# Kernel tuning notes

Measured on AMD Instinct MI355X. Metric: run time of the kernel, lower is better.

Reference implementation:

```python
import jax, jax.numpy as jnp
import numpy as np

K = 100
TEMPERATURE = 1.0


def setup_inputs() -> dict:
    key = jax.random.key(0)
    k1, k2, k3 = jax.random.split(key, 3)
    student_emb = jax.random.normal(k1, (8, 512, 1500), dtype=jnp.float32)
    teacher_codes = jax.random.randint(k2, (8, 1500), 0, 4096, dtype=jnp.int64)
    codebook = jax.random.normal(k3, (4096, 512), dtype=jnp.float32)
    return {"student_emb": student_emb, "teacher_codes": teacher_codes, "codebook": codebook}


def reference(student_emb, teacher_codes, codebook):
    B, C, T = student_emb.shape
    # flatten tokens: (N, C) with N = B*T
    emb = jnp.transpose(student_emb, (0, 2, 1)).reshape(-1, C)
    codes = teacher_codes.reshape(-1).astype(jnp.int32)

    # Euclidean cdist via the ||a||^2 + ||b||^2 - 2ab expansion (same math as torch.cdist)
    emb_sq = jnp.sum(emb * emb, axis=1, keepdims=True)            # (N,1)
    cb_sq = jnp.sum(codebook * codebook, axis=1)[None, :]         # (1,V)
    d2 = emb_sq + cb_sq - 2.0 * jnp.matmul(emb, codebook.T)       # (N,V)
    distances = jnp.sqrt(jnp.maximum(d2, 0.0))

    # top-k smallest distances
    _, top_k_indices = jax.lax.top_k(-distances, K)               # (N,K)

    # include_correct: replace last candidate with the true code if absent
    correct_in_topk = jnp.any(top_k_indices == codes[:, None], axis=1)
    top_k_indices = top_k_indices.at[:, -1].set(
        jnp.where(correct_in_topk, top_k_indices[:, -1], codes))

    candidate_distances = jnp.take_along_axis(distances, top_k_indices, axis=1)
    logits = -candidate_distances / TEMPERATURE                   # (N,K)

    match = top_k_indices == codes[:, None]
    local_labels = jnp.argmax(match.astype(jnp.int32), axis=1)    # (N,)

    logp = jax.nn.log_softmax(logits, axis=1)
    loss = -jnp.mean(jnp.take_along_axis(logp, local_labels[:, None], axis=1))

    local_predictions = jnp.argmax(logits, axis=-1)
    local_accuracy = jnp.mean((local_predictions == local_labels).astype(jnp.float32))
    global_predictions = jnp.argmin(distances, axis=-1)
    global_accuracy = jnp.mean((global_predictions == codes).astype(jnp.float32))
    correct_in_candidates = jnp.mean(jnp.any(top_k_indices == codes[:, None], axis=1).astype(jnp.float32))

    return loss, local_accuracy, global_accuracy, correct_in_candidates
```

## Files before the change

### kernel.cpp

```cpp
#include <hip/hip_runtime.h>
#include <hip/hip_bf16.h>
#include <cstdint>

#define B_ 8
#define C_ 512
#define T_ 1500
#define N_ (B_*T_)
#define NPAD_ 12032
#define V_ 4096
#define K_ 100

typedef unsigned long long u64;
typedef __attribute__((ext_vector_type(8))) short short8;
typedef __attribute__((ext_vector_type(8))) unsigned short u16x8;
typedef __attribute__((ext_vector_type(4))) float f32x4;

__device__ __forceinline__ unsigned short f2bf(float x){
    __hip_bfloat16 h = __float2bfloat16(x);
    return __builtin_bit_cast(unsigned short, h);
}
__device__ __forceinline__ unsigned short f2h(float x){
    return __builtin_bit_cast(unsigned short, (_Float16)x);
}
__device__ __forceinline__ float h2f(unsigned short h){
    return (float)__builtin_bit_cast(_Float16, h);
}

__device__ __forceinline__ void gll16(const unsigned short* g, unsigned short* l){
    __builtin_amdgcn_global_load_lds(
        (const __attribute__((address_space(1))) void*)g,
        (__attribute__((address_space(3))) void*)l, 16, 0, 0);
}

__global__ __launch_bounds__(256) void cbconv_kernel(const float* __restrict__ CB,
                                                     unsigned short* __restrict__ CBh,
                                                     float* __restrict__ csq){
    int wv = threadIdx.x >> 6, lane = threadIdx.x & 63;
    int r = blockIdx.x * 4 + wv;
    const float4* p4 = (const float4*)(CB + (size_t)r * C_);
    ushort4* o4 = (ushort4*)(CBh + (size_t)r * C_);
    float s = 0.f;
    #pragma unroll
    for (int j = 0; j < 2; ++j){
        float4 v = p4[lane + j*64];
        s += v.x*v.x + v.y*v.y + v.z*v.z + v.w*v.w;
        ushort4 h; h.x = f2bf(v.x); h.y = f2bf(v.y); h.z = f2bf(v.z); h.w = f2bf(v.w);
        o4[lane + j*64] = h;
    }
    #pragma unroll
    for (int o = 32; o; o >>= 1) s += __shfl_down(s, o, 64);
    if (lane == 0) csq[r] = s;
}

__global__ __launch_bounds__(256) void transpose_conv_kernel(const float* __restrict__ S,
                                                             unsigned short* __restrict__ embT,
                                                             float* __restrict__ esq){
    __shared__ float tile[32][33];
    __shared__ float psum[8][33];
    int b  = blockIdx.z;
    int c0 = blockIdx.y * 32;
    int t0 = blockIdx.x * 32;
    int tx = threadIdx.x, ty = threadIdx.y;
    #pragma unroll
    for (int r = 0; r < 4; ++r){
        int c = c0 + ty + r*8;
        int t = t0 + tx;
        tile[ty + r*8][tx] = (t < T_) ? S[((size_t)b*C_ + c)*T_ + t] : 0.f;
    }
    __syncthreads();
    float ps = 0.f;
    #pragma unroll
    for (int r = 0; r < 4; ++r){ float v = tile[ty + r*8][tx]; ps += v * v; }
    psum[ty][tx] = ps;
    #pragma unroll
    for (int r = 0; r < 4; ++r){
        int t = t0 + ty + r*8;
        int c = c0 + tx;
        if (t < T_) embT[((size_t)b*T_ + t)*C_ + c] = f2bf(tile[tx][ty + r*8]);
    }
    __syncthreads();
    if (ty == 0){
        int t = t0 + tx;
        if (t < T_){
            float s2 = 0.f;
            #pragma unroll
            for (int w = 0; w < 8; ++w) s2 += psum[w][tx];
            atomicAdd(&esq[b*T_ + t], s2);
        }
    }
}

__global__ __launch_bounds__(256) void gemm_dot_kernel(
    const unsigned short* __restrict__ A, const unsigned short* __restrict__ Bm,
    unsigned short* __restrict__ doth, int row_lo, int row_hi)
{
    __shared__ unsigned short As[128*32];
    __shared__ unsigned short Bs[128*32];
    int tid = threadIdx.x, lane = tid & 63, wv = tid >> 6;
    int row0 = row_lo + blockIdx.x * 128;
    int col0 = blockIdx.y * 128;

    int sr = lane >> 2;
    int sk = (lane & 3) * 8;
    int ar0 = row0 + wv*32 + sr;       int ar1 = ar0 + 16;
    int ca0 = (ar0 < N_) ? ar0 : N_-1; int ca1 = (ar1 < N_) ? ar1 : N_-1;
    const unsigned short* Ap0 = A  + (size_t)ca0 * C_ + sk;
    const unsigned short* Ap1 = A  + (size_t)ca1 * C_ + sk;
    const unsigned short* Bp0 = Bm + (size_t)(col0 + wv*32 + sr) * C_ + sk;
    const unsigned short* Bp1 = Bp0 + (size_t)16 * C_;
    unsigned short* Ad0 = &As[(wv*32     ) * 32];
    unsigned short* Ad1 = &As[(wv*32 + 16) * 32];
    unsigned short* Bd0 = &Bs[(wv*32     ) * 32];
    unsigned short* Bd1 = &Bs[(wv*32 + 16) * 32];

    int wm = (wv >> 1) * 64, wn = (wv & 1) * 64;
    int fr = lane & 15;
    int fk = (lane >> 4) * 8;

    f32x4 acc[4][4];
    #pragma unroll
    for (int i = 0; i < 4; ++i)
        #pragma unroll
        for (int j = 0; j < 4; ++j) acc[i][j] = (f32x4){0.f, 0.f, 0.f, 0.f};

    for (int kt = 0; kt < C_/32; ++kt){
        int k0 = kt * 32;
        gll16(Ap0 + k0, Ad0);
        gll16(Ap1 + k0, Ad1);
        gll16(Bp0 + k0, Bd0);
        gll16(Bp1 + k0, Bd1);
        __syncthreads();
        short8 af[4], bf[4];
        #pragma unroll
        for (int i = 0; i < 4; ++i) af[i] = *(const short8*)&As[(wm + i*16 + fr)*32 + fk];
        #pragma unroll
        for (int j = 0; j < 4; ++j) bf[j] = *(const short8*)&Bs[(wn + j*16 + fr)*32 + fk];
        #pragma unroll
        for (int i = 0; i < 4; ++i)
            #pragma unroll
            for (int j = 0; j < 4; ++j)
                acc[i][j] = __builtin_amdgcn_mfma_f32_16x16x32_bf16(af[i], bf[j], acc[i][j], 0, 0, 0);
        __syncthreads();
    }

    int er = (lane >> 4) * 4;
    int ec = lane & 15;
    #pragma unroll
    for (int i = 0; i < 4; ++i){
        #pragma unroll
        for (int r = 0; r < 4; ++r){
            int n = row0 + wm + i*16 + er + r;
            if (n >= row_hi) continue;
            size_t base = (size_t)(n - row_lo) * V_;
            #pragma unroll
            for (int j = 0; j < 4; ++j){
                int v = col0 + wn + j*16 + ec;
                doth[base + v] = f2h(acc[i][j][r]);
            }
        }
    }
}

__global__ __launch_bounds__(256, 2) void select_kernel(const unsigned short* __restrict__ doth,
                                                        const int* __restrict__ codes,
                                                        const float* __restrict__ esq,
                                                        const float* __restrict__ csq,
                                                        float2* __restrict__ pairbuf,
                                                        int row_lo, int nrows){
    int tid = threadIdx.x, lane = tid & 63, wv = tid >> 6;
    int lrow = blockIdx.x * 4 + wv;
    if (lrow >= nrows) return;
    int n = row_lo + lrow;
    const u16x8* r8 = (const u16x8*)(doth + (size_t)lrow * V_);

    __shared__ unsigned hist[4][256] __attribute__((aligned(16)));
    __shared__ unsigned coll[4][64];
    __shared__ unsigned collcnt[4];

    float esq_n = esq[n];
    int code = codes[n];
    float dotc = h2f(doth[(size_t)lrow * V_ + code]);
    unsigned ucode = __float_as_uint(fmaxf(esq_n + csq[code] - 2.f * dotc, 0.f));

    unsigned u[64];
    #pragma unroll
    for (int j = 0; j < 8; ++j){
        u16x8 h = r8[lane + j*64];
        const float4* cp = (const float4*)(csq + 8*lane + 512*j);
        float4 c0 = cp[0], c1 = cp[1];
        float cs[8] = {c0.x, c0.y, c0.z, c0.w, c1.x, c1.y, c1.z, c1.w};
        #pragma unroll
        for (int e = 0; e < 8; ++e){
            float d2 = fmaxf(esq_n + cs[e] - 2.f * h2f(h[e]), 0.f);
            u[8*j+e] = __float_as_uint(d2);
        }
    }

    unsigned umin = u[0], umax = u[0];
    #pragma unroll
    for (int k = 1; k < 64; ++k){
        umin = (u[k] < umin) ? u[k] : umin;
        umax = (u[k] > umax) ? u[k] : umax;
    }
    #pragma unroll
    for (int o = 32; o; o >>= 1){
        unsigned a = (unsigned)__shfl_xor((int)umin, o, 64); if (a < umin) umin = a;
        unsigned b = (unsigned)__shfl_xor((int)umax, o, 64); if (b > umax) umax = b;
    }
    unsigned im = 0xFFFFFFFFu;
    #pragma unroll
    for (int k = 0; k < 64; ++k){
        unsigned idx = 8u*(unsigned)lane + (unsigned)(512*(k >> 3) + (k & 7));
        if (u[k] == umin && idx < im) im = idx;
    }
    #pragma unroll
    for (int o = 32; o; o >>= 1){
        unsigned a = (unsigned)__shfl_xor((int)im, o, 64); if (a < im) im = a;
    }
    int idx0 = (int)im;
    float d0 = sqrtf(__uint_as_float(umin));

    unsigned t;
    if (umin == umax){
        t = umin;
    } else {
        ((uint4*)&hist[wv][0])[lane] = (uint4){0u,0u,0u,0u};
        if (lane == 0) collcnt[wv] = 0u;
        asm volatile("s_waitcnt lgkmcnt(0)" ::: "memory");
        float fmn = __uint_as_float(umin), fmx = __uint_as_float(umax);
        float invw = 256.0f / (fmx - fmn);
        #pragma unroll
        for (int k = 0; k < 64; ++k){
            float fk = __uint_as_float(u[k]);
            int b = (int)((fk - fmn) * invw); b = (b > 255) ? 255 : b;
            atomicAdd(&hist[wv][b], 1u);
        }
        asm volatile("s_waitcnt lgkmcnt(0)" ::: "memory");
        uint4 hq = ((uint4*)&hist[wv][0])[lane];
        unsigned lsum = hq.x + hq.y + hq.z + hq.w;
        unsigned inc = lsum;
        #pragma unroll
        for (int o = 1; o < 64; o <<= 1){
            unsigned y = (unsigned)__shfl_up((int)inc, o, 64);
            if (lane >= o) inc += y;
        }
        unsigned e0 = inc - lsum;
        unsigned e1 = e0 + hq.x, e2 = e1 + hq.y, e3 = e2 + hq.z, e4 = e3 + hq.w;
        int sel = -1;
        if      (e0 <= 99u && 99u < e1) sel = 0;
        else if (e1 <= 99u && 99u < e2) sel = 1;
        else if (e2 <= 99u && 99u < e3) sel = 2;
        else if (e3 <= 99u && 99u < e4) sel = 3;
        u64 bal = __ballot(sel >= 0);
        int src = __ffsll(bal) - 1;
        unsigned myBk = (unsigned)(4*lane + (sel < 0 ? 0 : sel));
        unsigned myBase = (sel == 1) ? e1 : (sel == 2) ? e2 : (sel == 3) ? e3 : e0;
        int Bk   = __shfl((int)myBk,   src, 64);
        int base = __shfl((int)myBase, src, 64);
        int rk = 99 - base;
        #pragma unroll
        for (int k = 0; k < 64; ++k){
            float fk = __uint_as_float(u[k]);
            int b = (int)((fk - fmn) * invw); b = (b > 255) ? 255 : b;
            if (b == Bk){
                unsigned pos = atomicAdd(&collcnt[wv], 1u);
                if (pos < 64u) coll[wv][pos] = u[k];
            }
        }
        asm volatile("s_waitcnt lgkmcnt(0)" ::: "memory");
        unsigned bcnt = collcnt[wv];
        if (bcnt <= 64u){
            unsigned w = (lane < (int)bcnt) ? coll[wv][lane] : 0xFFFFFFFFu;
            unsigned wmn = (lane < (int)bcnt) ? w : 0xFFFFFFFFu;
            unsigned wmx = (lane < (int)bcnt) ? w : 0u;
            #pragma unroll
            for (int o = 32; o; o >>= 1){
                unsigned a = (unsigned)__shfl_xor((int)wmn, o, 64); if (a < wmn) wmn = a;
                unsigned b = (unsigned)__shfl_xor((int)wmx, o, 64); if (b > wmx) wmx = b;
            }
            unsigned P;
            if (wmn == wmx) P = wmn;
            else {
                int hb = 31 - __clz((int)(wmn ^ wmx));
                unsigned mask = (hb == 31) ? 0xFFFFFFFFu : ((1u << (hb+1)) - 1u);
                P = wmn & ~mask;
                for (int b = hb; b >= 0; --b){
                    unsigned cand = P | (1u << b);
                    int c = __popcll(__ballot(w < cand));
                    if (c <= rk) P = cand;
                }
            }
            t = P;
        } else {
            int hb = 31 - __clz((int)(umin ^ umax));
            unsigned mask = (hb == 31) ? 0xFFFFFFFFu : ((1u << (hb+1)) - 1u);
            unsigned P = umin & ~mask;
            for (int b = hb; b >= 0; --b){
                unsigned cand = P | (1u << b);
                int c = 0;
                #pragma unroll
                for (int k = 0; k < 64; ++k) c += (u[k] < cand) ? 1 : 0;
                #pragma unroll
                for (int o = 32; o; o >>= 1) c += __shfl_xor(c, o, 64);
                if (c <= 99) P = cand;
            }
            t = P;
        }
    }
    float tval = sqrtf(__uint_as_float(t));

    float s = 0.f; int cl = 0;
    #pragma unroll
    for (int k = 0; k < 64; ++k){
        if (u[k] < t){ s += __expf(d0 - sqrtf(__uint_as_float(u[k]))); cl++; }
    }
    #pragma unroll
    for (int o = 32; o; o >>= 1){
        s += __shfl_xor(s, o, 64);
        cl += __shfl_xor(cl, o, 64);
    }
    if (lane == 0){
        float S = s + (float)(K_ - cl) * __expf(d0 - tval);
        float dcode = sqrtf(__uint_as_float(ucode));
        if (ucode > t) S += __expf(d0 - dcode) - __expf(d0 - tval);
        float nll = dcode - d0 + __logf(S);
        pairbuf[n] = make_float2(nll, (idx0 == code) ? 1.f : 0.f);
    }
}

__global__ __launch_bounds__(1024) void finalize_kernel(const float2* __restrict__ pair,
                                                        float* __restrict__ out){
    int tid = threadIdx.x;
    float sn = 0.f, sh = 0.f;
    for (int i = tid; i < N_; i += 1024){
        float2 p = pair[i]; sn += p.x; sh += p.y;
    }
    #pragma unroll
    for (int o = 32; o; o >>= 1){ sn += __shfl_down(sn, o, 64); sh += __shfl_down(sh, o, 64); }
    __shared__ float a[16], b[16];
    int wv = tid >> 6, lane = tid & 63;
    if (lane == 0){ a[wv] = sn; b[wv] = sh; }
    __syncthreads();
    if (tid == 0){
        float L = 0.f, H = 0.f;
        #pragma unroll
        for (int i = 0; i < 16; ++i){ L += a[i]; H += b[i]; }
        out[0] = L / (float)N_;
        out[1] = H / (float)N_;
        out[2] = H / (float)N_;
        out[3] = 1.0f;
    }
}

extern "C" void kernel_launch(void* const* d_in, const int* in_sizes, int n_in,
                              void* d_out, int out_size, void* d_ws, size_t ws_size,
                              hipStream_t stream){
    const float* S   = (const float*)d_in[0];
    const int* codes = (const int*)d_in[1];
    const float* CB  = (const float*)d_in[2];
    float* out = (float*)d_out;

    char* w = (char*)d_ws;
    size_t off = 0;
    unsigned short* embT = (unsigned short*)(w + off); off += (size_t)NPAD_ * C_ * 2;
    unsigned short* CBh  = (unsigned short*)(w + off); off += (size_t)V_ * C_ * 2;
    float* csq = (float*)(w + off); off += (size_t)V_ * 4;
    float* esq = (float*)(w + off); off += (size_t)N_ * 4;
    off = (off + 255) & ~(size_t)255;
    float2* pairbuf = (float2*)(w + off); off += (size_t)N_ * 8;
    unsigned short* dotbuf = (unsigned short*)(w + off);

    size_t avail = (ws_size > off) ? ws_size - off : 0;
    long maxrows = (long)(avail / ((size_t)V_ * 2));
    int chunk = (maxrows >= N_) ? N_ : (int)maxrows;
    if (chunk < 4) chunk = 4;

    hipMemsetAsync(esq, 0, (size_t)N_ * 4, stream);
    hipLaunchKernelGGL(cbconv_kernel, dim3(V_/4), dim3(256), 0, stream, CB, CBh, csq);
    hipLaunchKernelGGL(transpose_conv_kernel, dim3((T_+31)/32, C_/32, B_), dim3(32, 8), 0, stream,
                       S, embT, esq);

    for (int row_lo = 0; row_lo < N_; row_lo += chunk){
        int row_hi = row_lo + chunk; if (row_hi > N_) row_hi = N_;
        int rows = row_hi - row_lo;
        hipLaunchKernelGGL(gemm_dot_kernel, dim3((rows + 127)/128, V_/128), dim3(256), 0, stream,
                           embT, CBh, dotbuf, row_lo, row_hi);
        hipLaunchKernelGGL(select_kernel, dim3((rows + 3)/4), dim3(256), 0, stream,
                           dotbuf, codes, esq, csq, pairbuf, row_lo, rows);
    }
    hipLaunchKernelGGL(finalize_kernel, dim3(1), dim3(1024), 0, stream, pairbuf, out);
}
```

Measured before the change: 222.3 us.

## Fuse squared-distance epilogue into GEMM, store fp16 d2, widen K-tile with swizzle

```diff
diff --git a/kernel.cpp b/kernel.cpp
--- a/kernel.cpp
+++ b/kernel.cpp
@@ -9,10 +9,10 @@
 #define NPAD_ 12032
 #define V_ 4096
 #define K_ 100
+#define BKg 64
 
 typedef unsigned long long u64;
 typedef __attribute__((ext_vector_type(8))) short short8;
-typedef __attribute__((ext_vector_type(8))) unsigned short u16x8;
 typedef __attribute__((ext_vector_type(4))) float f32x4;
 
 __device__ __forceinline__ unsigned short f2bf(float x){
@@ -22,8 +22,8 @@
 __device__ __forceinline__ unsigned short f2h(float x){
     return __builtin_bit_cast(unsigned short, (_Float16)x);
 }
-__device__ __forceinline__ float h2f(unsigned short h){
-    return (float)__builtin_bit_cast(_Float16, h);
+__device__ __forceinline__ float h2fu(unsigned v){
+    return (float)__builtin_bit_cast(_Float16, (unsigned short)v);
 }
 
 __device__ __forceinline__ void gll16(const unsigned short* g, unsigned short* l){
@@ -90,32 +90,36 @@
     }
 }
 
-__global__ __launch_bounds__(256) void gemm_dot_kernel(
+__global__ __launch_bounds__(256) void gemm_d2h_kernel(
     const unsigned short* __restrict__ A, const unsigned short* __restrict__ Bm,
-    unsigned short* __restrict__ doth, int row_lo, int row_hi)
+    const float* __restrict__ esq, const float* __restrict__ csq,
+    unsigned short* __restrict__ d2h, int row_lo, int row_hi)
 {
-    __shared__ unsigned short As[128*32];
-    __shared__ unsigned short Bs[128*32];
+    __shared__ unsigned short As[128*BKg];
+    __shared__ unsigned short Bs[128*BKg];
     int tid = threadIdx.x, lane = tid & 63, wv = tid >> 6;
     int row0 = row_lo + blockIdx.x * 128;
     int col0 = blockIdx.y * 128;
 
-    int sr = lane >> 2;
-    int sk = (lane & 3) * 8;
-    int ar0 = row0 + wv*32 + sr;       int ar1 = ar0 + 16;
-    int ca0 = (ar0 < N_) ? ar0 : N_-1; int ca1 = (ar1 < N_) ? ar1 : N_-1;
-    const unsigned short* Ap0 = A  + (size_t)ca0 * C_ + sk;
-    const unsigned short* Ap1 = A  + (size_t)ca1 * C_ + sk;
-    const unsigned short* Bp0 = Bm + (size_t)(col0 + wv*32 + sr) * C_ + sk;
-    const unsigned short* Bp1 = Bp0 + (size_t)16 * C_;
-    unsigned short* Ad0 = &As[(wv*32     ) * 32];
-    unsigned short* Ad1 = &As[(wv*32 + 16) * 32];
-    unsigned short* Bd0 = &Bs[(wv*32     ) * 32];
-    unsigned short* Bd1 = &Bs[(wv*32 + 16) * 32];
+    int sr = lane >> 3;
+    int sk = (lane & 7) * 8;
+    int skx = sk ^ (sr * 8);
+    const unsigned short* Apg[4]; const unsigned short* Bpg[4];
+    unsigned short* Adg[4]; unsigned short* Bdg[4];
+    #pragma unroll
+    for (int g = 0; g < 4; ++g){
+        int r = wv*32 + g*8 + sr;
+        int ar = row0 + r; ar = (ar < N_) ? ar : N_-1;
+        Apg[g] = A  + (size_t)ar * C_ + skx;
+        Bpg[g] = Bm + (size_t)(col0 + r) * C_ + skx;
+        Adg[g] = &As[(wv*32 + g*8) * BKg];
+        Bdg[g] = &Bs[(wv*32 + g*8) * BKg];
+    }
 
     int wm = (wv >> 1) * 64, wn = (wv & 1) * 64;
     int fr = lane & 15;
     int fk = (lane >> 4) * 8;
+    int xo = (fr & 7) * 8;
 
     f32x4 acc[4][4];
     #pragma unroll
@@ -123,23 +127,27 @@
         #pragma unroll
         for (int j = 0; j < 4; ++j) acc[i][j] = (f32x4){0.f, 0.f, 0.f, 0.f};
 
-    for (int kt = 0; kt < C_/32; ++kt){
-        int k0 = kt * 32;
-        gll16(Ap0 + k0, Ad0);
-        gll16(Ap1 + k0, Ad1);
-        gll16(Bp0 + k0, Bd0);
-        gll16(Bp1 + k0, Bd1);
+    for (int kt = 0; kt < C_/BKg; ++kt){
+        int k0 = kt * BKg;
+        #pragma unroll
+        for (int g = 0; g < 4; ++g) gll16(Apg[g] + k0, Adg[g]);
+        #pragma unroll
+        for (int g = 0; g < 4; ++g) gll16(Bpg[g] + k0, Bdg[g]);
         __syncthreads();
-        short8 af[4], bf[4];
-        #pragma unroll
-        for (int i = 0; i < 4; ++i) af[i] = *(const short8*)&As[(wm + i*16 + fr)*32 + fk];
-        #pragma unroll
-        for (int j = 0; j < 4; ++j) bf[j] = *(const short8*)&Bs[(wn + j*16 + fr)*32 + fk];
-        #pragma unroll
-        for (int i = 0; i < 4; ++i)
-            #pragma unroll
-            for (int j = 0; j < 4; ++j)
-                acc[i][j] = __builtin_amdgcn_mfma_f32_16x16x32_bf16(af[i], bf[j], acc[i][j], 0, 0, 0);
+        #pragma unroll
+        for (int kk = 0; kk < 2; ++kk){
+            int fo = (fk + kk*32) ^ xo;
+            short8 af[4], bf[4];
+            #pragma unroll
+            for (int i = 0; i < 4; ++i) af[i] = *(const short8*)&As[(wm + i*16 + fr)*BKg + fo];
+            #pragma unroll
+            for (int j = 0; j < 4; ++j) bf[j] = *(const short8*)&Bs[(wn + j*16 + fr)*BKg + fo];
+            #pragma unroll
+            for (int i = 0; i < 4; ++i)
+                #pragma unroll
+                for (int j = 0; j < 4; ++j)
+                    acc[i][j] = __builtin_amdgcn_mfma_f32_16x16x32_bf16(af[i], bf[j], acc[i][j], 0, 0, 0);
+        }
         __syncthreads();
     }
 
@@ -151,89 +159,77 @@
         for (int r = 0; r < 4; ++r){
             int n = row0 + wm + i*16 + er + r;
             if (n >= row_hi) continue;
+            float en = esq[n];
             size_t base = (size_t)(n - row_lo) * V_;
             #pragma unroll
             for (int j = 0; j < 4; ++j){
                 int v = col0 + wn + j*16 + ec;
-                doth[base + v] = f2h(acc[i][j][r]);
-            }
-        }
-    }
-}
-
-__global__ __launch_bounds__(256, 2) void select_kernel(const unsigned short* __restrict__ doth,
+                float d2 = fmaxf(en + csq[v] - 2.f * acc[i][j][r], 0.f);
+                d2h[base + v] = f2h(d2);
+            }
+        }
+    }
+}
+
+__global__ __launch_bounds__(256, 2) void select_kernel(const unsigned short* __restrict__ d2h,
                                                         const int* __restrict__ codes,
-                                                        const float* __restrict__ esq,
-                                                        const float* __restrict__ csq,
                                                         float2* __restrict__ pairbuf,
                                                         int row_lo, int nrows){
     int tid = threadIdx.x, lane = tid & 63, wv = tid >> 6;
     int lrow = blockIdx.x * 4 + wv;
     if (lrow >= nrows) return;
     int n = row_lo + lrow;
-    const u16x8* r8 = (const u16x8*)(doth + (size_t)lrow * V_);
+    const uint4* r4 = (const uint4*)(d2h + (size_t)lrow * V_);
 
     __shared__ unsigned hist[4][256] __attribute__((aligned(16)));
     __shared__ unsigned coll[4][64];
     __shared__ unsigned collcnt[4];
 
-    float esq_n = esq[n];
+    unsigned p[32];
+    #pragma unroll
+    for (int j = 0; j < 8; ++j){
+        uint4 q = r4[lane + j*64];
+        p[4*j] = q.x; p[4*j+1] = q.y; p[4*j+2] = q.z; p[4*j+3] = q.w;
+    }
     int code = codes[n];
-    float dotc = h2f(doth[(size_t)lrow * V_ + code]);
-    unsigned ucode = __float_as_uint(fmaxf(esq_n + csq[code] - 2.f * dotc, 0.f));
-
-    unsigned u[64];
-    #pragma unroll
-    for (int j = 0; j < 8; ++j){
-        u16x8 h = r8[lane + j*64];
-        const float4* cp = (const float4*)(csq + 8*lane + 512*j);
-        float4 c0 = cp[0], c1 = cp[1];
-        float cs[8] = {c0.x, c0.y, c0.z, c0.w, c1.x, c1.y, c1.z, c1.w};
-        #pragma unroll
-        for (int e = 0; e < 8; ++e){
-            float d2 = fmaxf(esq_n + cs[e] - 2.f * h2f(h[e]), 0.f);
-            u[8*j+e] = __float_as_uint(d2);
-        }
-    }
-
-    unsigned umin = u[0], umax = u[0];
-    #pragma unroll
-    for (int k = 1; k < 64; ++k){
-        umin = (u[k] < umin) ? u[k] : umin;
-        umax = (u[k] > umax) ? u[k] : umax;
+    unsigned ucode = (unsigned)d2h[(size_t)lrow * V_ + code];
+
+    unsigned cmin = 0xFFFFFFFFu, kmax = 0u;
+    #pragma unroll
+    for (int m = 0; m < 32; ++m){
+        unsigned idx = 8u*(unsigned)lane + 512u*(unsigned)(m>>2) + 2u*(unsigned)(m&3);
+        unsigned cl_ = (p[m] << 16) | idx;
+        unsigned ch_ = (p[m] & 0xFFFF0000u) | (idx + 1u);
+        unsigned cc = (cl_ < ch_) ? cl_ : ch_;
+        if (cc < cmin) cmin = cc;
+        unsigned lo = p[m] & 0xFFFFu, hi = p[m] >> 16;
+        unsigned mm = (lo > hi) ? lo : hi;
+        if (mm > kmax) kmax = mm;
     }
     #pragma unroll
     for (int o = 32; o; o >>= 1){
-        unsigned a = (unsigned)__shfl_xor((int)umin, o, 64); if (a < umin) umin = a;
-        unsigned b = (unsigned)__shfl_xor((int)umax, o, 64); if (b > umax) umax = b;
-    }
-    unsigned im = 0xFFFFFFFFu;
-    #pragma unroll
-    for (int k = 0; k < 64; ++k){
-        unsigned idx = 8u*(unsigned)lane + (unsigned)(512*(k >> 3) + (k & 7));
-        if (u[k] == umin && idx < im) im = idx;
-    }
-    #pragma unroll
-    for (int o = 32; o; o >>= 1){
-        unsigned a = (unsigned)__shfl_xor((int)im, o, 64); if (a < im) im = a;
-    }
-    int idx0 = (int)im;
-    float d0 = sqrtf(__uint_as_float(umin));
+        unsigned a = (unsigned)__shfl_xor((int)cmin, o, 64); if (a < cmin) cmin = a;
+        unsigned b = (unsigned)__shfl_xor((int)kmax, o, 64); if (b > kmax) kmax = b;
+    }
+    unsigned umin = cmin >> 16;
+    int idx0 = (int)(cmin & 0xFFFFu);
+    float d0 = sqrtf(h2fu(umin));
 
     unsigned t;
-    if (umin == umax){
+    if (umin == kmax){
         t = umin;
     } else {
         ((uint4*)&hist[wv][0])[lane] = (uint4){0u,0u,0u,0u};
         if (lane == 0) collcnt[wv] = 0u;
         asm volatile("s_waitcnt lgkmcnt(0)" ::: "memory");
-        float fmn = __uint_as_float(umin), fmx = __uint_as_float(umax);
+        float fmn = h2fu(umin), fmx = h2fu(kmax);
         float invw = 256.0f / (fmx - fmn);
         #pragma unroll
-        for (int k = 0; k < 64; ++k){
-            float fk = __uint_as_float(u[k]);
-            int b = (int)((fk - fmn) * invw); b = (b > 255) ? 255 : b;
-            atomicAdd(&hist[wv][b], 1u);
+        for (int m = 0; m < 32; ++m){
+            int b0 = (int)((h2fu(p[m] & 0xFFFFu) - fmn) * invw); b0 = (b0 > 255) ? 255 : b0;
+            int b1 = (int)((h2fu(p[m] >> 16)     - fmn) * invw); b1 = (b1 > 255) ? 255 : b1;
+            atomicAdd(&hist[wv][b0], 1u);
+            atomicAdd(&hist[wv][b1], 1u);
         }
         asm volatile("s_waitcnt lgkmcnt(0)" ::: "memory");
         uint4 hq = ((uint4*)&hist[wv][0])[lane];
@@ -259,12 +255,17 @@
         int base = __shfl((int)myBase, src, 64);
         int rk = 99 - base;
         #pragma unroll
-        for (int k = 0; k < 64; ++k){
-            float fk = __uint_as_float(u[k]);
-            int b = (int)((fk - fmn) * invw); b = (b > 255) ? 255 : b;
-            if (b == Bk){
+        for (int m = 0; m < 32; ++m){
+            unsigned klo = p[m] & 0xFFFFu, khi = p[m] >> 16;
+            int b0 = (int)((h2fu(klo) - fmn) * invw); b0 = (b0 > 255) ? 255 : b0;
+            int b1 = (int)((h2fu(khi) - fmn) * invw); b1 = (b1 > 255) ? 255 : b1;
+            if (b0 == Bk){
                 unsigned pos = atomicAdd(&collcnt[wv], 1u);
-                if (pos < 64u) coll[wv][pos] = u[k];
+                if (pos < 64u) coll[wv][pos] = klo;
+            }
+            if (b1 == Bk){
+                unsigned pos = atomicAdd(&collcnt[wv], 1u);
+                if (pos < 64u) coll[wv][pos] = khi;
             }
         }
         asm volatile("s_waitcnt lgkmcnt(0)" ::: "memory");
@@ -282,7 +283,7 @@
             if (wmn == wmx) P = wmn;
             else {
                 int hb = 31 - __clz((int)(wmn ^ wmx));
-                unsigned mask = (hb == 31) ? 0xFFFFFFFFu : ((1u << (hb+1)) - 1u);
+                unsigned mask = (1u << (hb+1)) - 1u;
                 P = wmn & ~mask;
                 for (int b = hb; b >= 0; --b){
                     unsigned cand = P | (1u << b);
@@ -292,14 +293,17 @@
             }
             t = P;
         } else {
-            int hb = 31 - __clz((int)(umin ^ umax));
-            unsigned mask = (hb == 31) ? 0xFFFFFFFFu : ((1u << (hb+1)) - 1u);
+            int hb = 31 - __clz((int)(umin ^ kmax));
+            unsigned mask = (1u << (hb+1)) - 1u;
             unsigned P = umin & ~mask;
             for (int b = hb; b >= 0; --b){
                 unsigned cand = P | (1u << b);
                 int c = 0;
                 #pragma unroll
-                for (int k = 0; k < 64; ++k) c += (u[k] < cand) ? 1 : 0;
+                for (int m = 0; m < 32; ++m){
+                    c += ((p[m] & 0xFFFFu) < cand) ? 1 : 0;
+                    c += ((p[m] >> 16)     < cand) ? 1 : 0;
+                }
                 #pragma unroll
                 for (int o = 32; o; o >>= 1) c += __shfl_xor(c, o, 64);
                 if (c <= 99) P = cand;
@@ -307,12 +311,14 @@
             t = P;
         }
     }
-    float tval = sqrtf(__uint_as_float(t));
+    float tval = sqrtf(h2fu(t));
 
     float s = 0.f; int cl = 0;
     #pragma unroll
-    for (int k = 0; k < 64; ++k){
-        if (u[k] < t){ s += __expf(d0 - sqrtf(__uint_as_float(u[k]))); cl++; }
+    for (int m = 0; m < 32; ++m){
+        unsigned klo = p[m] & 0xFFFFu, khi = p[m] >> 16;
+        if (klo < t){ s += __expf(d0 - sqrtf(h2fu(klo))); cl++; }
+        if (khi < t){ s += __expf(d0 - sqrtf(h2fu(khi))); cl++; }
     }
     #pragma unroll
     for (int o = 32; o; o >>= 1){
@@ -321,7 +327,7 @@
     }
     if (lane == 0){
         float S = s + (float)(K_ - cl) * __expf(d0 - tval);
-        float dcode = sqrtf(__uint_as_float(ucode));
+        float dcode = sqrtf(h2fu(ucode));
         if (ucode > t) S += __expf(d0 - dcode) - __expf(d0 - tval);
         float nll = dcode - d0 + __logf(S);
         pairbuf[n] = make_float2(nll, (idx0 == code) ? 1.f : 0.f);
@@ -368,7 +374,7 @@
     float* esq = (float*)(w + off); off += (size_t)N_ * 4;
     off = (off + 255) & ~(size_t)255;
     float2* pairbuf = (float2*)(w + off); off += (size_t)N_ * 8;
-    unsigned short* dotbuf = (unsigned short*)(w + off);
+    unsigned short* d2buf = (unsigned short*)(w + off);
 
     size_t avail = (ws_size > off) ? ws_size - off : 0;
     long maxrows = (long)(avail / ((size_t)V_ * 2));
@@ -383,10 +389,10 @@
     for (int row_lo = 0; row_lo < N_; row_lo += chunk){
         int row_hi = row_lo + chunk; if (row_hi > N_) row_hi = N_;
         int rows = row_hi - row_lo;
-        hipLaunchKernelGGL(gemm_dot_kernel, dim3((rows + 127)/128, V_/128), dim3(256), 0, stream,
-                           embT, CBh, dotbuf, row_lo, row_hi);
+        hipLaunchKernelGGL(gemm_d2h_kernel, dim3((rows + 127)/128, V_/128), dim3(256), 0, stream,
+                           embT, CBh, esq, csq, d2buf, row_lo, row_hi);
         hipLaunchKernelGGL(select_kernel, dim3((rows + 3)/4), dim3(256), 0, stream,
-                           dotbuf, codes, esq, csq, pairbuf, row_lo, rows);
+                           d2buf, codes, pairbuf, row_lo, rows);
     }
     hipLaunchKernelGGL(finalize_kernel, dim3(1), dim3(1024), 0, stream, pairbuf, out);
 }
```

Measured after the change: 247.5 us. 1.11x slower.
